# Kernel optimization log

Hardware: AMD Instinct MI355X
Metric: run time of the kernel (lower is better)

Reference implementation:

```python
import jax, jax.numpy as jnp
import numpy as np

B, S, D, H, DH = 2, 2048, 1024, 16, 64
LN_EPS = 1e-5

def _layernorm(x, g, b):
    mu = jnp.mean(x, axis=-1, keepdims=True)
    var = jnp.mean(jnp.square(x - mu), axis=-1, keepdims=True)
    return (x - mu) * jax.lax.rsqrt(var + LN_EPS) * g + b

def setup_inputs() -> dict:
    key = jax.random.key(0)
    ks = jax.random.split(key, 12)
    s = 0.02
    return {
        'x': jax.random.normal(ks[0], (B, S, D), jnp.float32),
        'attention_mask': jnp.zeros((B, S), jnp.bool_),
        'Wq': jax.random.normal(ks[1], (H, D, DH), jnp.float32) * s,
        'bq': jnp.zeros((H, DH), jnp.float32),
        'Wk': jax.random.normal(ks[2], (H, D, DH), jnp.float32) * s,
        'bk': jnp.zeros((H, DH), jnp.float32),
        'Wv': jax.random.normal(ks[3], (H, D, DH), jnp.float32) * s,
        'bv': jnp.zeros((H, DH), jnp.float32),
        'ln_g': jnp.ones((D,), jnp.float32),
        'ln_b': jnp.zeros((D,), jnp.float32),
        'W1': jax.random.normal(ks[4], (D, 4 * D), jnp.float32) * s,
        'b1': jnp.zeros((4 * D,), jnp.float32),
        'W2': jax.random.normal(ks[5], (4 * D, D), jnp.float32) * s,
        'b2': jnp.zeros((D,), jnp.float32),
    }

def reference(x, attention_mask, Wq, bq, Wk, bk, Wv, bv, ln_g, ln_b, W1, b1, W2, b2):
    # NOTE: source has a typo bug ('attentoin_score'), so the attention_mask is
    # computed-then-discarded; softmax is applied to the UNMASKED scaled scores.
    dh = Wq.shape[-1]
    q = jnp.einsum('bsd,hde->bhse', x, Wq) + bq[:, None, :]  # [B,H,S,dh]
    k = jnp.einsum('bsd,hde->bhse', x, Wk) + bk[:, None, :]
    v = jnp.einsum('bsd,hde->bhse', x, Wv) + bv[:, None, :]
    scores = jnp.einsum('bhse,bhte->bhst', q, k) / jnp.sqrt(jnp.float32(dh))
    attn = jax.nn.softmax(scores, axis=-1)
    o = jnp.einsum('bhst,bhte->bhse', attn, v)  # [B,H,S,dh]
    b_, h_, s_, e_ = o.shape
    # concat heads along last dim == transpose then reshape
    mha = jnp.transpose(o, (0, 2, 1, 3)).reshape(b_, s_, h_ * e_)
    h1 = _layernorm(x + mha, ln_g, ln_b)
    ffn = jax.nn.relu(h1 @ W1 + b1) @ W2 + b2
    return _layernorm(h1 + ffn, ln_g, ln_b)
```

## Files before the change

### kernel.cpp

```cpp
#include <hip/hip_runtime.h>

#define DEVI __device__ __forceinline__

typedef __attribute__((ext_vector_type(8))) __bf16 bf16x8;
typedef __attribute__((ext_vector_type(4))) float f32x4;
typedef __attribute__((ext_vector_type(4))) unsigned short u16x4;
typedef __attribute__((ext_vector_type(8))) unsigned short u16x8;

static DEVI unsigned short f2bf(float f) {
  unsigned int i = __float_as_uint(f);
  i += 0x7fffu + ((i >> 16) & 1u);
  return (unsigned short)(i >> 16);
}

static DEVI unsigned short f2bfh(float f) {
  union { __bf16 h; unsigned short u; } c;
  c.h = (__bf16)f;
  return c.u;
}

static DEVI f32x4 mfma16x16x32(bf16x8 a, bf16x8 b, f32x4 c) {
  return __builtin_amdgcn_mfma_f32_16x16x32_bf16(a, b, c, 0, 0, 0);
}

static DEVI void async_ld16(const void* g, void* lds) {
  __builtin_amdgcn_global_load_lds(
      (const __attribute__((address_space(1))) void*)g,
      (__attribute__((address_space(3))) void*)lds, 16, 0, 0);
}

template <int BN, int OUT_MODE, bool RELU>
static DEVI void gemm_bt_core(const unsigned short* __restrict__ A, int lda,
                              const unsigned short* __restrict__ Bt, int ldb,
                              int K, int m0, int n0,
                              const float* __restrict__ bias,
                              void* __restrict__ Cp, int ldc,
                              const float* __restrict__ bq,
                              const float* __restrict__ bk,
                              const float* __restrict__ bv,
                              unsigned short* __restrict__ qo,
                              unsigned short* __restrict__ ko,
                              unsigned short* __restrict__ vo) {
  constexpr int MT = (BN == 128) ? 4 : 2;
  constexpr int NT = 4;
  __shared__ __align__(16) unsigned short As[128 * 32];
  __shared__ __align__(16) unsigned short Bs[BN * 32];

  const int tid = threadIdx.x;
  const int w = tid >> 6, l = tid & 63;
  const int lr = l & 15, lq = l >> 4;
  const int wm0 = (BN == 128) ? ((w >> 1) * 64) : (w * 32);
  const int wn0 = (BN == 128) ? ((w & 1) * 64) : 0;
  const int lrow = l >> 2;
  const int lcol = (l & 3) * 8;

  f32x4 acc[MT][NT];
#pragma unroll
  for (int i = 0; i < MT; ++i)
#pragma unroll
    for (int j = 0; j < NT; ++j) acc[i][j] = (f32x4){0.f, 0.f, 0.f, 0.f};

  for (int kb = 0; kb < K; kb += 32) {
#pragma unroll
    for (int p = 0; p < 2; ++p) {
      const int r0 = p * 64 + w * 16;
      async_ld16(A + (size_t)(m0 + r0 + lrow) * lda + kb + lcol, As + r0 * 32);
    }
#pragma unroll
    for (int p = 0; p < BN / 64; ++p) {
      const int r0 = p * 64 + w * 16;
      async_ld16(Bt + (size_t)(n0 + r0 + lrow) * ldb + kb + lcol, Bs + r0 * 32);
    }
    __syncthreads();

    bf16x8 af[MT], bfr[NT];
#pragma unroll
    for (int mt = 0; mt < MT; ++mt)
      af[mt] = *(const bf16x8*)(As + (wm0 + mt * 16 + lr) * 32 + lq * 8);
#pragma unroll
    for (int nt = 0; nt < NT; ++nt)
      bfr[nt] = *(const bf16x8*)(Bs + (wn0 + nt * 16 + lr) * 32 + lq * 8);
#pragma unroll
    for (int mt = 0; mt < MT; ++mt)
#pragma unroll
      for (int nt = 0; nt < NT; ++nt)
        acc[mt][nt] = mfma16x16x32(af[mt], bfr[nt], acc[mt][nt]);
    __syncthreads();
  }

#pragma unroll
  for (int mt = 0; mt < MT; ++mt) {
    const int grow = m0 + wm0 + mt * 16 + lq * 4;
#pragma unroll
    for (int nt = 0; nt < NT; ++nt) {
      const int gcol = n0 + wn0 + nt * 16 + lr;
      if (OUT_MODE == 2) {
        const int which = gcol >> 10;
        const int h = (gcol >> 6) & 15;
        const int e = gcol & 63;
        const float* bp = (which == 0) ? bq : (which == 1) ? bk : bv;
        const float bvv = bp[gcol & 1023];
        unsigned short* op = (which == 0) ? qo : (which == 1) ? ko : vo;
#pragma unroll
        for (int r = 0; r < 4; ++r) {
          const int row = grow + r;
          const int b_ = row >> 11, s_ = row & 2047;
          const size_t base = (size_t)((b_ << 4) + h) * 131072 + (size_t)s_ * 64;
          if (which == 1) {
            const int o = e >> 3;
            const int pos = (((o ^ (s_ & 7)) << 3) | (e & 7));
            op[base + pos] = f2bf((acc[mt][nt][r] + bvv) * 0.18033688011112f);
          } else {
            op[base + e] = f2bf(acc[mt][nt][r] + bvv);
          }
        }
      } else if (OUT_MODE == 3) {
#pragma unroll
        for (int r = 0; r < 4; ++r)
          ((unsigned short*)Cp)[(size_t)(grow + r) * ldc + gcol] =
              f2bf(acc[mt][nt][r]);
      } else {
        const float bvv = bias[gcol];
#pragma unroll
        for (int r = 0; r < 4; ++r) {
          float val = acc[mt][nt][r] + bvv;
          if (RELU) val = fmaxf(val, 0.f);
          if (OUT_MODE == 1)
            ((unsigned short*)Cp)[(size_t)(grow + r) * ldc + gcol] = f2bf(val);
          else
            ((float*)Cp)[(size_t)(grow + r) * ldc + gcol] = val;
        }
      }
    }
  }
}

__global__ __launch_bounds__(256) void k_gemm_qkv(
    const unsigned short* __restrict__ xb, const unsigned short* __restrict__ Wt,
    const float* __restrict__ bq, const float* __restrict__ bk,
    const float* __restrict__ bv, unsigned short* __restrict__ qo,
    unsigned short* __restrict__ ko, unsigned short* __restrict__ vo) {
  gemm_bt_core<128, 2, false>(xb, 1024, Wt, 1024, 1024, blockIdx.x * 128,
                              blockIdx.y * 128, nullptr, nullptr, 0, bq, bk, bv,
                              qo, ko, vo);
}

__global__ __launch_bounds__(256) void k_ffn1(
    const unsigned short* __restrict__ h1b, const unsigned short* __restrict__ W1t,
    const float* __restrict__ b1, unsigned short* __restrict__ f1) {
  gemm_bt_core<128, 1, true>(h1b, 1024, W1t, 1024, 1024, blockIdx.x * 128,
                             blockIdx.y * 128, b1, f1, 4096, nullptr, nullptr,
                             nullptr, nullptr, nullptr, nullptr);
}

__global__ __launch_bounds__(256) void k_ffn2(
    const unsigned short* __restrict__ f1, const unsigned short* __restrict__ W2t,
    unsigned short* __restrict__ p0, unsigned short* __restrict__ p1) {
  const int z = blockIdx.z;
  unsigned short* p = z ? p1 : p0;
  gemm_bt_core<64, 3, false>(f1 + z * 2048, 4096, W2t + z * 2048, 4096, 2048,
                             blockIdx.x * 128, blockIdx.y * 64, nullptr, p, 1024,
                             nullptr, nullptr, nullptr, nullptr, nullptr,
                             nullptr);
}

__global__ __launch_bounds__(256) void k_cvt(const float* __restrict__ src,
                                             unsigned short* __restrict__ dst) {
  const size_t i = ((size_t)blockIdx.x * 256 + threadIdx.x) * 4;
  f32x4 v = *(const f32x4*)(src + i);
  u16x4 pk;
#pragma unroll
  for (int j = 0; j < 4; ++j) pk[j] = f2bf(v[j]);
  *(u16x4*)(dst + i) = pk;
}

static DEVI void tr64(const float* __restrict__ s, int sld,
                      unsigned short* __restrict__ d, int dld) {
  __shared__ float t[64][65];
  const int tr = threadIdx.x >> 4;
  const int tc4 = (threadIdx.x & 15) * 4;
#pragma unroll
  for (int i = 0; i < 4; ++i) {
    f32x4 v = *(const f32x4*)(s + (size_t)(i * 16 + tr) * sld + tc4);
#pragma unroll
    for (int j = 0; j < 4; ++j) t[i * 16 + tr][tc4 + j] = v[j];
  }
  __syncthreads();
#pragma unroll
  for (int i = 0; i < 4; ++i) {
    const int c = i * 16 + tr;
    u16x4 pk;
#pragma unroll
    for (int j = 0; j < 4; ++j) pk[j] = f2bf(t[tc4 + j][c]);
    *(u16x4*)(d + (size_t)c * dld + tc4) = pk;
  }
}

__global__ __launch_bounds__(256) void k_tw(const float* __restrict__ src,
                                            unsigned short* __restrict__ dst,
                                            int C) {
  const int R = (int)gridDim.x * 64;
  const int r0 = blockIdx.x * 64, c0 = blockIdx.y * 64;
  tr64(src + (size_t)r0 * C + c0, C, dst + (size_t)c0 * R + r0, R);
}

__global__ __launch_bounds__(256) void k_twqkv(const float* __restrict__ Wq,
                                               const float* __restrict__ Wk,
                                               const float* __restrict__ Wv,
                                               unsigned short* __restrict__ dst) {
  const int which = blockIdx.y >> 4, h = blockIdx.y & 15;
  const float* W = (which == 0) ? Wq : (which == 1) ? Wk : Wv;
  const float* s = W + (size_t)h * 65536;
  unsigned short* d = dst + (size_t)(which * 1024 + h * 64) * 1024;
  const int r0 = blockIdx.x * 64;
  tr64(s + (size_t)r0 * 64, 64, d + r0, 1024);
}

__global__ __launch_bounds__(256) void k_vprep(const unsigned short* __restrict__ vb,
                                               unsigned short* __restrict__ vp) {
  const int bh = blockIdx.y, t = blockIdx.x;
  __shared__ unsigned short tl[64][72];
  const int tid = threadIdx.x;
  const size_t base = (size_t)bh * 131072;
  const int kr = tid >> 3, oc = tid & 7;
#pragma unroll
  for (int p = 0; p < 2; ++p) {
    const int key = p * 32 + kr;
    *(u16x8*)&tl[key][oc * 8] =
        *(const u16x8*)(vb + base + (size_t)(t * 64 + key) * 64 + oc * 8);
  }
  __syncthreads();
#pragma unroll
  for (int p = 0; p < 2; ++p) {
    const int dh = p * 32 + kr;
    const int ok = oc ^ (dh & 7);
    u16x8 pk;
#pragma unroll
    for (int j = 0; j < 8; ++j) {
      const int kap = ok * 8 + j;
      const int key = (kap & 3) * 16 + (kap >> 2);
      pk[j] = tl[key][dh];
    }
    *(u16x8*)(vp + base + (size_t)dh * 2048 + t * 64 + oc * 8) = pk;
  }
}

__global__ __launch_bounds__(512) void k_attn(
    const unsigned short* __restrict__ q, const unsigned short* __restrict__ ks,
    const unsigned short* __restrict__ vp, float* __restrict__ mha) {
  const int bid = blockIdx.x;
  const int bh = (bid & 7) * 4 + ((bid >> 3) >> 4);
  const int qt = (bid >> 3) & 15;
  const int b = bh >> 4, h = bh & 15;
  const int tid = threadIdx.x;
  const int w = tid >> 6, l = tid & 63;
  const int lr = l & 15, lq = l >> 4, l7 = lr & 7;

  __shared__ __align__(16) unsigned short Ks[2][64 * 64];
  __shared__ __align__(16) unsigned short Vt[2][64 * 64];
  __shared__ __align__(16) unsigned short Ps[8][16][72];

  const size_t bho = (size_t)bh * 131072;
  const int q0 = qt * 128 + w * 16;

  bf16x8 qf0, qf1;
  {
    const unsigned short* qp = q + bho + (size_t)(q0 + lr) * 64 + lq * 8;
    qf0 = *(const bf16x8*)qp;
    qf1 = *(const bf16x8*)(qp + 32);
  }

  f32x4 l_acc[4];
  f32x4 o[4];
#pragma unroll
  for (int i = 0; i < 4; ++i) {
    l_acc[i] = (f32x4){0.f, 0.f, 0.f, 0.f};
    o[i] = (f32x4){0.f, 0.f, 0.f, 0.f};
  }

  const unsigned short* kg = ks + bho;
  const unsigned short* vg = vp + bho;
  const int srow = l >> 3, scol = (l & 7) * 8;
  const int r0 = w * 8;

  async_ld16(kg + (size_t)(r0 + srow) * 64 + scol, &Ks[0][r0 * 64]);
  async_ld16(vg + (size_t)(r0 + srow) * 2048 + scol, &Vt[0][r0 * 64]);
  __syncthreads();

  for (int kt = 0; kt < 32; ++kt) {
    const int cur = kt & 1, nxt = cur ^ 1;
    if (kt + 1 < 32) {
      const int k1 = (kt + 1) * 64;
      async_ld16(kg + (size_t)(k1 + r0 + srow) * 64 + scol, &Ks[nxt][r0 * 64]);
      async_ld16(vg + (size_t)(r0 + srow) * 2048 + k1 + scol, &Vt[nxt][r0 * 64]);
    }

    bf16x8 kf[4][2];
#pragma unroll
    for (int ct = 0; ct < 4; ++ct)
#pragma unroll
      for (int hh = 0; hh < 2; ++hh)
        kf[ct][hh] = *(const bf16x8*)&Ks[cur][(ct * 16 + lr) * 64 +
                                             (((hh << 2) | lq) ^ l7) * 8];
    f32x4 s[4];
#pragma unroll
    for (int ct = 0; ct < 4; ++ct) {
      f32x4 t = {0.f, 0.f, 0.f, 0.f};
      t = mfma16x16x32(qf0, kf[ct][0], t);
      t = mfma16x16x32(qf1, kf[ct][1], t);
      s[ct] = t;
    }

#pragma unroll
    for (int r = 0; r < 4; ++r) {
      f32x4 pe;
#pragma unroll
      for (int ct = 0; ct < 4; ++ct)
        pe[ct] = __builtin_amdgcn_exp2f(s[ct][r]);
      l_acc[r] += pe;
      u16x4 pk;
#pragma unroll
      for (int ct = 0; ct < 4; ++ct) pk[ct] = f2bfh(pe[ct]);
      *(u16x4*)&Ps[w][lq * 4 + r][lr * 4] = pk;
    }
    __asm__ volatile("" ::: "memory");

    bf16x8 vf[4][2];
#pragma unroll
    for (int dt = 0; dt < 4; ++dt)
#pragma unroll
      for (int hh = 0; hh < 2; ++hh)
        vf[dt][hh] = *(const bf16x8*)&Vt[cur][(dt * 16 + lr) * 64 +
                                             (((hh << 2) | lq) ^ l7) * 8];
    bf16x8 pf0 = *(const bf16x8*)&Ps[w][lr][lq * 8];
    bf16x8 pf1 = *(const bf16x8*)&Ps[w][lr][32 + lq * 8];
#pragma unroll
    for (int dt = 0; dt < 4; ++dt) {
      o[dt] = mfma16x16x32(pf0, vf[dt][0], o[dt]);
      o[dt] = mfma16x16x32(pf1, vf[dt][1], o[dt]);
    }
    __syncthreads();
  }

#pragma unroll
  for (int r = 0; r < 4; ++r) {
    f32x4 la = l_acc[r];
    float sd = la[0] + la[1] + la[2] + la[3];
    sd += __shfl_xor(sd, 1);
    sd += __shfl_xor(sd, 2);
    sd += __shfl_xor(sd, 4);
    sd += __shfl_xor(sd, 8);
    const float inv = 1.f / sd;
    float* op = mha + ((size_t)b * 2048 + q0 + lq * 4 + r) * 1024 + h * 64 + lr;
    op[0] = o[0][r] * inv;
    op[16] = o[1][r] * inv;
    op[32] = o[2][r] * inv;
    op[48] = o[3][r] * inv;
  }
}

__global__ __launch_bounds__(256) void k_add_ln(const float* __restrict__ a,
                                                const float* __restrict__ b,
                                                const float* __restrict__ g,
                                                const float* __restrict__ be,
                                                float* __restrict__ out,
                                                unsigned short* __restrict__ outb) {
  const int row = blockIdx.x;
  const int tid = threadIdx.x;
  const size_t base = (size_t)row * 1024 + tid * 4;
  f32x4 va = *(const f32x4*)(a + base);
  f32x4 vb = *(const f32x4*)(b + base);
  f32x4 xx;
  float s = 0.f, q = 0.f;
#pragma unroll
  for (int i = 0; i < 4; ++i) {
    xx[i] = va[i] + vb[i];
    s += xx[i];
    q += xx[i] * xx[i];
  }
#pragma unroll
  for (int off = 1; off < 64; off <<= 1) {
    s += __shfl_xor(s, off);
    q += __shfl_xor(q, off);
  }
  __shared__ float ss[4], qs[4];
  const int w = tid >> 6;
  if ((tid & 63) == 0) { ss[w] = s; qs[w] = q; }
  __syncthreads();
  s = ss[0] + ss[1] + ss[2] + ss[3];
  q = qs[0] + qs[1] + qs[2] + qs[3];
  const float mean = s * (1.f / 1024.f);
  const float var = q * (1.f / 1024.f) - mean * mean;
  const float rstd = rsqrtf(var + 1e-5f);
  f32x4 vg = *(const f32x4*)(g + tid * 4);
  f32x4 vbe = *(const f32x4*)(be + tid * 4);
  f32x4 ov;
#pragma unroll
  for (int i = 0; i < 4; ++i) ov[i] = (xx[i] - mean) * rstd * vg[i] + vbe[i];
  *(f32x4*)(out + base) = ov;
  if (outb) {
    u16x4 pk;
#pragma unroll
    for (int i = 0; i < 4; ++i) pk[i] = f2bf(ov[i]);
    *(u16x4*)(outb + base) = pk;
  }
}

__global__ __launch_bounds__(256) void k_add_ln3(
    const float* __restrict__ a, const unsigned short* __restrict__ p0,
    const unsigned short* __restrict__ p1, const float* __restrict__ cb,
    const float* __restrict__ g, const float* __restrict__ be,
    float* __restrict__ out) {
  const int row = blockIdx.x;
  const int tid = threadIdx.x;
  const size_t base = (size_t)row * 1024 + tid * 4;
  f32x4 va = *(const f32x4*)(a + base);
  u16x4 u0 = *(const u16x4*)(p0 + base);
  u16x4 u1 = *(const u16x4*)(p1 + base);
  f32x4 vcb = *(const f32x4*)(cb + tid * 4);
  f32x4 xx;
  float s = 0.f, q = 0.f;
#pragma unroll
  for (int i = 0; i < 4; ++i) {
    const float f0 = __uint_as_float((unsigned int)u0[i] << 16);
    const float f1 = __uint_as_float((unsigned int)u1[i] << 16);
    xx[i] = va[i] + f0 + f1 + vcb[i];
    s += xx[i];
    q += xx[i] * xx[i];
  }
#pragma unroll
  for (int off = 1; off < 64; off <<= 1) {
    s += __shfl_xor(s, off);
    q += __shfl_xor(q, off);
  }
  __shared__ float ss[4], qs[4];
  const int w = tid >> 6;
  if ((tid & 63) == 0) { ss[w] = s; qs[w] = q; }
  __syncthreads();
  s = ss[0] + ss[1] + ss[2] + ss[3];
  q = qs[0] + qs[1] + qs[2] + qs[3];
  const float mean = s * (1.f / 1024.f);
  const float var = q * (1.f / 1024.f) - mean * mean;
  const float rstd = rsqrtf(var + 1e-5f);
  f32x4 vg = *(const f32x4*)(g + tid * 4);
  f32x4 vbe = *(const f32x4*)(be + tid * 4);
  f32x4 ov;
#pragma unroll
  for (int i = 0; i < 4; ++i) ov[i] = (xx[i] - mean) * rstd * vg[i] + vbe[i];
  *(f32x4*)(out + base) = ov;
}

extern "C" void kernel_launch(void* const* d_in, const int* in_sizes, int n_in,
                              void* d_out, int out_size, void* d_ws,
                              size_t ws_size, hipStream_t stream) {
  const float* x = (const float*)d_in[0];
  const float* Wq = (const float*)d_in[2];
  const float* bq = (const float*)d_in[3];
  const float* Wk = (const float*)d_in[4];
  const float* bk = (const float*)d_in[5];
  const float* Wv = (const float*)d_in[6];
  const float* bv = (const float*)d_in[7];
  const float* lg = (const float*)d_in[8];
  const float* lb = (const float*)d_in[9];
  const float* W1 = (const float*)d_in[10];
  const float* b1 = (const float*)d_in[11];
  const float* W2 = (const float*)d_in[12];
  const float* b2 = (const float*)d_in[13];

  char* ws = (char*)d_ws;
  const size_t MB = 1024 * 1024;
  unsigned short* qb = (unsigned short*)(ws + 0);
  unsigned short* kb = (unsigned short*)(ws + 8 * MB);
  unsigned short* vb = (unsigned short*)(ws + 16 * MB);
  unsigned short* vp = (unsigned short*)(ws + 24 * MB);
  unsigned short* w2t = (unsigned short*)(ws + 0);
  unsigned short* f1 = (unsigned short*)(ws + 8 * MB);
  unsigned short* xb = (unsigned short*)(ws + 40 * MB);
  float* mha = (float*)(ws + 40 * MB);
  unsigned short* p1 = (unsigned short*)(ws + 40 * MB);
  float* h1 = (float*)(ws + 56 * MB);
  unsigned short* h1b = (unsigned short*)(ws + 72 * MB);
  unsigned short* p0 = (unsigned short*)(ws + 72 * MB);
  unsigned short* wqkvt = (unsigned short*)(ws + 80 * MB);
  unsigned short* w1t = (unsigned short*)(ws + 86 * MB);

  k_cvt<<<dim3(4096), 256, 0, stream>>>(x, xb);
  k_twqkv<<<dim3(16, 48), 256, 0, stream>>>(Wq, Wk, Wv, wqkvt);
  k_tw<<<dim3(16, 64), 256, 0, stream>>>(W1, w1t, 4096);

  k_gemm_qkv<<<dim3(32, 24), 256, 0, stream>>>(xb, wqkvt, bq, bk, bv, qb, kb, vb);
  k_vprep<<<dim3(32, 32), 256, 0, stream>>>(vb, vp);
  k_attn<<<dim3(512), 512, 0, stream>>>(qb, kb, vp, mha);

  k_tw<<<dim3(64, 16), 256, 0, stream>>>(W2, w2t, 1024);
  k_add_ln<<<dim3(4096), 256, 0, stream>>>(x, mha, lg, lb, h1, h1b);
  k_ffn1<<<dim3(32, 32), 256, 0, stream>>>(h1b, w1t, b1, f1);
  k_ffn2<<<dim3(32, 16, 2), 256, 0, stream>>>(f1, w2t, p0, p1);
  k_add_ln3<<<dim3(4096), 256, 0, stream>>>(h1, p0, p1, b2, lg, lb,
                                            (float*)d_out);
}
```

Measured before the change: 329.1 us.

## Double GEMM K-tile with swizzled LDS, fuse V repack into QKV epilogue, drop fp32 h1

The shared GEMM core now stages 64-wide K slices per barrier pair instead of 32, using an XOR-swizzled LDS layout to avoid bank conflicts, which halves the number of loop iterations and syncs. The QKV GEMM epilogue writes V directly in the permuted, swizzled layout the attention kernel expects, so the separate k_vprep kernel and its intermediate buffer are removed. The first layernorm now writes only a bf16 copy of h1, and the final residual add reads that bf16 copy, cutting memory traffic at the cost of some precision in the residual path. Workspace offsets are reorganised to match.

```diff
diff --git a/kernel.cpp b/kernel.cpp
--- a/kernel.cpp
+++ b/kernel.cpp
@@ -17,6 +17,10 @@
   union { __bf16 h; unsigned short u; } c;
   c.h = (__bf16)f;
   return c.u;
+}
+
+static DEVI float bf2f(unsigned short u) {
+  return __uint_as_float((unsigned int)u << 16);
 }
 
 static DEVI f32x4 mfma16x16x32(bf16x8 a, bf16x8 b, f32x4 c) {
@@ -43,16 +47,16 @@
                               unsigned short* __restrict__ vo) {
   constexpr int MT = (BN == 128) ? 4 : 2;
   constexpr int NT = 4;
-  __shared__ __align__(16) unsigned short As[128 * 32];
-  __shared__ __align__(16) unsigned short Bs[BN * 32];
+  __shared__ __align__(16) unsigned short As[128 * 64];
+  __shared__ __align__(16) unsigned short Bs[BN * 64];
 
   const int tid = threadIdx.x;
   const int w = tid >> 6, l = tid & 63;
   const int lr = l & 15, lq = l >> 4;
   const int wm0 = (BN == 128) ? ((w >> 1) * 64) : (w * 32);
   const int wn0 = (BN == 128) ? ((w & 1) * 64) : 0;
-  const int lrow = l >> 2;
-  const int lcol = (l & 3) * 8;
+  const int srw = l >> 3;
+  const int sc = ((l & 7) ^ (((l >> 3) & 1) << 2)) * 8;
 
   f32x4 acc[MT][NT];
 #pragma unroll
@@ -60,31 +64,40 @@
 #pragma unroll
     for (int j = 0; j < NT; ++j) acc[i][j] = (f32x4){0.f, 0.f, 0.f, 0.f};
 
-  for (int kb = 0; kb < K; kb += 32) {
-#pragma unroll
-    for (int p = 0; p < 2; ++p) {
-      const int r0 = p * 64 + w * 16;
-      async_ld16(A + (size_t)(m0 + r0 + lrow) * lda + kb + lcol, As + r0 * 32);
-    }
-#pragma unroll
-    for (int p = 0; p < BN / 64; ++p) {
-      const int r0 = p * 64 + w * 16;
-      async_ld16(Bt + (size_t)(n0 + r0 + lrow) * ldb + kb + lcol, Bs + r0 * 32);
+  for (int kb = 0; kb < K; kb += 64) {
+#pragma unroll
+    for (int p = 0; p < 4; ++p) {
+      const int r0 = w * 32 + p * 8;
+      async_ld16(A + (size_t)(m0 + r0 + srw) * lda + kb + sc, As + r0 * 64);
+    }
+#pragma unroll
+    for (int p = 0; p < BN / 32; ++p) {
+      const int r0 = (BN == 128 ? w * 32 : w * 16) + p * 8;
+      async_ld16(Bt + (size_t)(n0 + r0 + srw) * ldb + kb + sc, Bs + r0 * 64);
     }
     __syncthreads();
 
-    bf16x8 af[MT], bfr[NT];
-#pragma unroll
-    for (int mt = 0; mt < MT; ++mt)
-      af[mt] = *(const bf16x8*)(As + (wm0 + mt * 16 + lr) * 32 + lq * 8);
-#pragma unroll
-    for (int nt = 0; nt < NT; ++nt)
-      bfr[nt] = *(const bf16x8*)(Bs + (wn0 + nt * 16 + lr) * 32 + lq * 8);
-#pragma unroll
-    for (int mt = 0; mt < MT; ++mt)
-#pragma unroll
-      for (int nt = 0; nt < NT; ++nt)
-        acc[mt][nt] = mfma16x16x32(af[mt], bfr[nt], acc[mt][nt]);
+#pragma unroll
+    for (int h = 0; h < 2; ++h) {
+      bf16x8 af[MT], bfr[NT];
+#pragma unroll
+      for (int mt = 0; mt < MT; ++mt) {
+        const int row = wm0 + mt * 16 + lr;
+        af[mt] =
+            *(const bf16x8*)(As + row * 64 + ((h ^ (row & 1)) << 5) + lq * 8);
+      }
+#pragma unroll
+      for (int nt = 0; nt < NT; ++nt) {
+        const int row = wn0 + nt * 16 + lr;
+        bfr[nt] =
+            *(const bf16x8*)(Bs + row * 64 + ((h ^ (row & 1)) << 5) + lq * 8);
+      }
+#pragma unroll
+      for (int mt = 0; mt < MT; ++mt)
+#pragma unroll
+        for (int nt = 0; nt < NT; ++nt)
+          acc[mt][nt] = mfma16x16x32(af[mt], bfr[nt], acc[mt][nt]);
+    }
     __syncthreads();
   }
 
@@ -100,18 +113,23 @@
         const int e = gcol & 63;
         const float* bp = (which == 0) ? bq : (which == 1) ? bk : bv;
         const float bvv = bp[gcol & 1023];
-        unsigned short* op = (which == 0) ? qo : (which == 1) ? ko : vo;
 #pragma unroll
         for (int r = 0; r < 4; ++r) {
           const int row = grow + r;
           const int b_ = row >> 11, s_ = row & 2047;
-          const size_t base = (size_t)((b_ << 4) + h) * 131072 + (size_t)s_ * 64;
-          if (which == 1) {
+          const size_t base = (size_t)((b_ << 4) + h) * 131072;
+          const float val = acc[mt][nt][r] + bvv;
+          if (which == 0) {
+            qo[base + (size_t)s_ * 64 + e] = f2bf(val);
+          } else if (which == 1) {
             const int o = e >> 3;
             const int pos = (((o ^ (s_ & 7)) << 3) | (e & 7));
-            op[base + pos] = f2bf((acc[mt][nt][r] + bvv) * 0.18033688011112f);
+            ko[base + (size_t)s_ * 64 + pos] = f2bf(val * 0.18033688011112f);
           } else {
-            op[base + e] = f2bf(acc[mt][nt][r] + bvv);
+            const int t = s_ >> 6, k64 = s_ & 63;
+            const int kap = (k64 & 15) * 4 + (k64 >> 4);
+            const int pos = (((kap >> 3) ^ (e & 7)) << 3) | (kap & 7);
+            vo[base + (size_t)e * 2048 + t * 64 + pos] = f2bf(val);
           }
         }
       } else if (OUT_MODE == 3) {
@@ -214,35 +232,6 @@
   unsigned short* d = dst + (size_t)(which * 1024 + h * 64) * 1024;
   const int r0 = blockIdx.x * 64;
   tr64(s + (size_t)r0 * 64, 64, d + r0, 1024);
-}
-
-__global__ __launch_bounds__(256) void k_vprep(const unsigned short* __restrict__ vb,
-                                               unsigned short* __restrict__ vp) {
-  const int bh = blockIdx.y, t = blockIdx.x;
-  __shared__ unsigned short tl[64][72];
-  const int tid = threadIdx.x;
-  const size_t base = (size_t)bh * 131072;
-  const int kr = tid >> 3, oc = tid & 7;
-#pragma unroll
-  for (int p = 0; p < 2; ++p) {
-    const int key = p * 32 + kr;
-    *(u16x8*)&tl[key][oc * 8] =
-        *(const u16x8*)(vb + base + (size_t)(t * 64 + key) * 64 + oc * 8);
-  }
-  __syncthreads();
-#pragma unroll
-  for (int p = 0; p < 2; ++p) {
-    const int dh = p * 32 + kr;
-    const int ok = oc ^ (dh & 7);
-    u16x8 pk;
-#pragma unroll
-    for (int j = 0; j < 8; ++j) {
-      const int kap = ok * 8 + j;
-      const int key = (kap & 3) * 16 + (kap >> 2);
-      pk[j] = tl[key][dh];
-    }
-    *(u16x8*)(vp + base + (size_t)dh * 2048 + t * 64 + oc * 8) = pk;
-  }
 }
 
 __global__ __launch_bounds__(512) void k_attn(
@@ -363,7 +352,6 @@
                                                 const float* __restrict__ b,
                                                 const float* __restrict__ g,
                                                 const float* __restrict__ be,
-                                                float* __restrict__ out,
                                                 unsigned short* __restrict__ outb) {
   const int row = blockIdx.x;
   const int tid = threadIdx.x;
@@ -394,27 +382,22 @@
   const float rstd = rsqrtf(var + 1e-5f);
   f32x4 vg = *(const f32x4*)(g + tid * 4);
   f32x4 vbe = *(const f32x4*)(be + tid * 4);
-  f32x4 ov;
-#pragma unroll
-  for (int i = 0; i < 4; ++i) ov[i] = (xx[i] - mean) * rstd * vg[i] + vbe[i];
-  *(f32x4*)(out + base) = ov;
-  if (outb) {
-    u16x4 pk;
-#pragma unroll
-    for (int i = 0; i < 4; ++i) pk[i] = f2bf(ov[i]);
-    *(u16x4*)(outb + base) = pk;
-  }
+  u16x4 pk;
+#pragma unroll
+  for (int i = 0; i < 4; ++i)
+    pk[i] = f2bf((xx[i] - mean) * rstd * vg[i] + vbe[i]);
+  *(u16x4*)(outb + base) = pk;
 }
 
 __global__ __launch_bounds__(256) void k_add_ln3(
-    const float* __restrict__ a, const unsigned short* __restrict__ p0,
+    const unsigned short* __restrict__ h1b, const unsigned short* __restrict__ p0,
     const unsigned short* __restrict__ p1, const float* __restrict__ cb,
     const float* __restrict__ g, const float* __restrict__ be,
     float* __restrict__ out) {
   const int row = blockIdx.x;
   const int tid = threadIdx.x;
   const size_t base = (size_t)row * 1024 + tid * 4;
-  f32x4 va = *(const f32x4*)(a + base);
+  u16x4 uh = *(const u16x4*)(h1b + base);
   u16x4 u0 = *(const u16x4*)(p0 + base);
   u16x4 u1 = *(const u16x4*)(p1 + base);
   f32x4 vcb = *(const f32x4*)(cb + tid * 4);
@@ -422,9 +405,7 @@
   float s = 0.f, q = 0.f;
 #pragma unroll
   for (int i = 0; i < 4; ++i) {
-    const float f0 = __uint_as_float((unsigned int)u0[i] << 16);
-    const float f1 = __uint_as_float((unsigned int)u1[i] << 16);
-    xx[i] = va[i] + f0 + f1 + vcb[i];
+    xx[i] = bf2f(uh[i]) + bf2f(u0[i]) + bf2f(u1[i]) + vcb[i];
     s += xx[i];
     q += xx[i] * xx[i];
   }
@@ -471,31 +452,27 @@
   const size_t MB = 1024 * 1024;
   unsigned short* qb = (unsigned short*)(ws + 0);
   unsigned short* kb = (unsigned short*)(ws + 8 * MB);
-  unsigned short* vb = (unsigned short*)(ws + 16 * MB);
-  unsigned short* vp = (unsigned short*)(ws + 24 * MB);
-  unsigned short* w2t = (unsigned short*)(ws + 0);
-  unsigned short* f1 = (unsigned short*)(ws + 8 * MB);
+  unsigned short* vp = (unsigned short*)(ws + 16 * MB);
+  unsigned short* f1 = (unsigned short*)(ws + 0);
+  float* mha = (float*)(ws + 32 * MB);
+  unsigned short* p0 = (unsigned short*)(ws + 32 * MB);
   unsigned short* xb = (unsigned short*)(ws + 40 * MB);
-  float* mha = (float*)(ws + 40 * MB);
   unsigned short* p1 = (unsigned short*)(ws + 40 * MB);
-  float* h1 = (float*)(ws + 56 * MB);
-  unsigned short* h1b = (unsigned short*)(ws + 72 * MB);
-  unsigned short* p0 = (unsigned short*)(ws + 72 * MB);
-  unsigned short* wqkvt = (unsigned short*)(ws + 80 * MB);
-  unsigned short* w1t = (unsigned short*)(ws + 86 * MB);
+  unsigned short* h1b = (unsigned short*)(ws + 48 * MB);
+  unsigned short* wqkvt = (unsigned short*)(ws + 56 * MB);
+  unsigned short* w1t = (unsigned short*)(ws + 62 * MB);
+  unsigned short* w2t = (unsigned short*)(ws + 70 * MB);
 
   k_cvt<<<dim3(4096), 256, 0, stream>>>(x, xb);
   k_twqkv<<<dim3(16, 48), 256, 0, stream>>>(Wq, Wk, Wv, wqkvt);
   k_tw<<<dim3(16, 64), 256, 0, stream>>>(W1, w1t, 4096);
-
-  k_gemm_qkv<<<dim3(32, 24), 256, 0, stream>>>(xb, wqkvt, bq, bk, bv, qb, kb, vb);
-  k_vprep<<<dim3(32, 32), 256, 0, stream>>>(vb, vp);
+  k_tw<<<dim3(64, 16), 256, 0, stream>>>(W2, w2t, 1024);
+
+  k_gemm_qkv<<<dim3(32, 24), 256, 0, stream>>>(xb, wqkvt, bq, bk, bv, qb, kb, vp);
   k_attn<<<dim3(512), 512, 0, stream>>>(qb, kb, vp, mha);
-
-  k_tw<<<dim3(64, 16), 256, 0, stream>>>(W2, w2t, 1024);
-  k_add_ln<<<dim3(4096), 256, 0, stream>>>(x, mha, lg, lb, h1, h1b);
+  k_add_ln<<<dim3(4096), 256, 0, stream>>>(x, mha, lg, lb, h1b);
   k_ffn1<<<dim3(32, 32), 256, 0, stream>>>(h1b, w1t, b1, f1);
   k_ffn2<<<dim3(32, 16, 2), 256, 0, stream>>>(f1, w2t, p0, p1);
-  k_add_ln3<<<dim3(4096), 256, 0, stream>>>(h1, p0, p1, b2, lg, lb,
+  k_add_ln3<<<dim3(4096), 256, 0, stream>>>(h1b, p0, p1, b2, lg, lb,
                                             (float*)d_out);
 }
```

Result: slower. 356.2 us (+8.3%).
